# Optimization experiments

Measured on AMD Instinct MI355X. Metric: run time of the kernel, lower is better.

## Reference

```python
import jax, jax.numpy as jnp
import numpy as np

D_MODEL = 1024
NUM_HEADS = 16
D_K = D_MODEL // NUM_HEADS


def setup_inputs() -> dict:
    key = jax.random.key(0)
    ks = jax.random.split(key, 12)
    B, S = 2, 2048
    s = 1.0 / np.sqrt(D_MODEL)
    inp = {
        "query": jax.random.normal(ks[0], (B, S, D_MODEL), jnp.float32),
        "key": jax.random.normal(ks[1], (B, S, D_MODEL), jnp.float32),
        "value": jax.random.normal(ks[2], (B, S, D_MODEL), jnp.float32),
        "Wq": jax.random.normal(ks[3], (D_MODEL, D_MODEL), jnp.float32) * s,
        "bq": jax.random.normal(ks[4], (D_MODEL,), jnp.float32) * s,
        "Wk": jax.random.normal(ks[5], (D_MODEL, D_MODEL), jnp.float32) * s,
        "bk": jax.random.normal(ks[6], (D_MODEL,), jnp.float32) * s,
        "Wv": jax.random.normal(ks[7], (D_MODEL, D_MODEL), jnp.float32) * s,
        "bv": jax.random.normal(ks[8], (D_MODEL,), jnp.float32) * s,
        "Wo": jax.random.normal(ks[9], (D_MODEL, D_MODEL), jnp.float32) * s,
        "bo": jax.random.normal(ks[10], (D_MODEL,), jnp.float32) * s,
    }
    return inp


def _split_heads(x):
    B, S, _ = x.shape
    return x.reshape(B, S, NUM_HEADS, D_K).transpose(0, 2, 1, 3)  # [B,H,S,Dk]


def reference(query, key, value, Wq, bq, Wk, bk, Wv, bv, Wo, bo):
    # Linear projections (torch Linear: x @ W.T + b)
    Q = _split_heads(query @ Wq.T + bq)
    K = _split_heads(key @ Wk.T + bk)
    V = _split_heads(value @ Wv.T + bv)
    scale = 1.0 / jnp.sqrt(jnp.asarray(D_K, Q.dtype))
    scores = jnp.einsum('bhqd,bhkd->bhqk', Q, K) * scale  # [B,H,S,S]
    attn = jax.nn.softmax(scores, axis=-1)
    # dropout is identity in eval mode
    x = jnp.einsum('bhqk,bhkd->bhqd', attn, V)
    B, H, S, Dk = x.shape
    x = x.transpose(0, 2, 1, 3).reshape(B, S, H * Dk)
    return x @ Wo.T + bo
```

## Files before the change

kernel.cpp:

```cpp
#include <hip/hip_runtime.h>
#include <hip/hip_bf16.h>

typedef __bf16 bf16;
typedef __attribute__((ext_vector_type(4))) __bf16 bf16x4;
typedef __attribute__((ext_vector_type(8))) __bf16 bf16x8;
typedef __attribute__((ext_vector_type(4))) float f32x4;
typedef __attribute__((ext_vector_type(16))) float f32x16;
typedef unsigned int u32;

#define D_MODEL 1024
#define NHEADS 16
#define DK 64
#define BATCH 2
#define SEQ 2048
#define NTOK (BATCH * SEQ)

#define QSCALE 0.18033688011112042f
#define DEFER_THR 8.0f

__device__ __forceinline__ u32 cvtpk_bf16(float lo, float hi) {
  u32 r;
  asm("v_cvt_pk_bf16_f32 %0, %1, %2" : "=v"(r) : "v"(lo), "v"(hi));
  return r;
}
__device__ __forceinline__ void plswap(u32& a, u32& b) {
  asm("v_permlane32_swap_b32 %0, %1" : "+v"(a), "+v"(b));
}
__device__ __forceinline__ float fast_exp2(float x) {
#if __has_builtin(__builtin_amdgcn_exp2f)
  return __builtin_amdgcn_exp2f(x);
#else
  return exp2f(x);
#endif
}
__device__ __forceinline__ float xhalf_max(float x) {
  return fmaxf(x, __shfl_xor(x, 32));
}
__device__ __forceinline__ float xhalf_add(float x) {
  return x + __shfl_xor(x, 32);
}

__device__ __forceinline__ int frag_off_q(int s, int d) {
  return ((s >> 5) << 11) + ((d >> 4) << 9) + ((((d >> 3) & 1) * 32 + (s & 31)) << 3) + (d & 7);
}
__device__ __forceinline__ int frag_off_k(int s, int d) {
  return ((s >> 6) << 12) + ((((s >> 5) & 1) * 4 + (d >> 4)) << 9) +
         ((((d >> 3) & 1) * 32 + (s & 31)) << 3) + (d & 7);
}
__device__ __forceinline__ int frag_off_v(int s, int d) {
  return ((s >> 6) << 12) + (((d >> 5) * 4 + ((s >> 4) & 3)) << 9) +
         ((((s >> 3) & 1) * 32 + (d & 31)) << 3) + (s & 7);
}

__global__ __launch_bounds__(256) void cvt3_kernel(
    const float* __restrict__ s0, const float* __restrict__ s1, const float* __restrict__ s2,
    bf16* __restrict__ d0, bf16* __restrict__ d1, bf16* __restrict__ d2, int n4) {
  int i = blockIdx.x * blockDim.x + threadIdx.x;
  if (i >= n4) return;
  const float* s = blockIdx.y == 0 ? s0 : blockIdx.y == 1 ? s1 : s2;
  bf16* d = blockIdx.y == 0 ? d0 : blockIdx.y == 1 ? d1 : d2;
  float4 v = reinterpret_cast<const float4*>(s)[i];
  bf16x4 o;
  o[0] = (bf16)v.x; o[1] = (bf16)v.y; o[2] = (bf16)v.z; o[3] = (bf16)v.w;
  reinterpret_cast<bf16x4*>(d)[i] = o;
}

__global__ __launch_bounds__(256) void cvt4_kernel(
    const float* __restrict__ s0, const float* __restrict__ s1,
    const float* __restrict__ s2, const float* __restrict__ s3,
    bf16* __restrict__ d0, bf16* __restrict__ d1, bf16* __restrict__ d2, bf16* __restrict__ d3,
    int n4) {
  int i = blockIdx.x * blockDim.x + threadIdx.x;
  if (i >= n4) return;
  const float* s = blockIdx.y == 0 ? s0 : blockIdx.y == 1 ? s1 : blockIdx.y == 2 ? s2 : s3;
  bf16* d = blockIdx.y == 0 ? d0 : blockIdx.y == 1 ? d1 : blockIdx.y == 2 ? d2 : d3;
  float4 v = reinterpret_cast<const float4*>(s)[i];
  bf16x4 o;
  o[0] = (bf16)v.x; o[1] = (bf16)v.y; o[2] = (bf16)v.z; o[3] = (bf16)v.w;
  reinterpret_cast<bf16x4*>(d)[i] = o;
}

#define ASYNC_COPY16(gptr, lptr)                                                \
  __builtin_amdgcn_global_load_lds(                                             \
      (__attribute__((address_space(1))) void*)(gptr),                          \
      (__attribute__((address_space(3))) void*)(lptr), 16, 0, 0)

struct ProjArgs {
  const bf16* A[3];
  const bf16* W[3];
  const float* bias[3];
  bf16* out[3];
};

__global__ __launch_bounds__(256) void gemm_proj(ProjArgs pa, int K) {
  __shared__ bf16 As[128][32];
  __shared__ bf16 Bs[128][32];
  const int z = blockIdx.z;
  const bf16* A = pa.A[z];
  const bf16* Bw = pa.W[z];
  const int m0 = blockIdx.x * 128;
  const int n0 = blockIdx.y * 128;

  const int t = threadIdx.x;
  const int wave = t >> 6;
  const int lane = t & 63;
  const int wr = (wave >> 1) * 64;
  const int wc = (wave & 1) * 64;
  const int r4 = lane >> 2;
  const int c8 = (lane & 3) * 8;
  const int fr = lane & 15;
  const int fk = (lane >> 4) * 8;

  f32x4 acc[4][4] = {};

  for (int k0 = 0; k0 < K; k0 += 32) {
    ASYNC_COPY16(&A[(size_t)(m0 + wave * 16 + r4) * K + k0 + c8], &As[wave * 16][0]);
    ASYNC_COPY16(&A[(size_t)(m0 + 64 + wave * 16 + r4) * K + k0 + c8], &As[64 + wave * 16][0]);
    ASYNC_COPY16(&Bw[(size_t)(n0 + wave * 16 + r4) * K + k0 + c8], &Bs[wave * 16][0]);
    ASYNC_COPY16(&Bw[(size_t)(n0 + 64 + wave * 16 + r4) * K + k0 + c8], &Bs[64 + wave * 16][0]);
    __syncthreads();

    bf16x8 af[4], bfr[4];
#pragma unroll
    for (int m = 0; m < 4; m++)
      af[m] = *reinterpret_cast<const bf16x8*>(&As[wr + m * 16 + fr][fk]);
#pragma unroll
    for (int n = 0; n < 4; n++)
      bfr[n] = *reinterpret_cast<const bf16x8*>(&Bs[wc + n * 16 + fr][fk]);
#pragma unroll
    for (int m = 0; m < 4; m++)
#pragma unroll
      for (int n = 0; n < 4; n++)
        acc[m][n] = __builtin_amdgcn_mfma_f32_16x16x32_bf16(af[m], bfr[n], acc[m][n], 0, 0, 0);
    __syncthreads();
  }

  const float scale = (z == 0) ? QSCALE : 1.0f;
  const float* bias = pa.bias[z];
  bf16* out = pa.out[z];
#pragma unroll
  for (int m = 0; m < 4; m++) {
#pragma unroll
    for (int n = 0; n < 4; n++) {
      const int col = n0 + wc + n * 16 + fr;
      const float bv = bias[col];
#pragma unroll
      for (int j = 0; j < 4; j++) {
        const int row = m0 + wr + m * 16 + (lane >> 4) * 4 + j;
        const float v = (acc[m][n][j] + bv) * scale;
        const int b = row >> 11;
        const int s = row & (SEQ - 1);
        const int h = col >> 6;
        const int d = col & (DK - 1);
        const size_t base = (size_t)(b * NHEADS + h) * SEQ * DK;
        int off;
        if (z == 0)      off = frag_off_q(s, d);
        else if (z == 1) off = frag_off_k(s, d);
        else             off = frag_off_v(s, d);
        out[base + off] = (bf16)v;
      }
    }
  }
}

__global__ __launch_bounds__(256) void gemm_out(
    const bf16* __restrict__ A, const bf16* __restrict__ Bw,
    const float* __restrict__ bias, float* __restrict__ out, int K) {
  __shared__ bf16 As[128][32];
  __shared__ bf16 Bs[128][32];
  const int m0 = blockIdx.x * 128;
  const int n0 = blockIdx.y * 128;

  const int t = threadIdx.x;
  const int wave = t >> 6;
  const int lane = t & 63;
  const int wr = (wave >> 1) * 64;
  const int wc = (wave & 1) * 64;
  const int r4 = lane >> 2;
  const int c8 = (lane & 3) * 8;
  const int fr = lane & 15;
  const int fk = (lane >> 4) * 8;

  f32x4 acc[4][4] = {};

  for (int k0 = 0; k0 < K; k0 += 32) {
    ASYNC_COPY16(&A[(size_t)(m0 + wave * 16 + r4) * K + k0 + c8], &As[wave * 16][0]);
    ASYNC_COPY16(&A[(size_t)(m0 + 64 + wave * 16 + r4) * K + k0 + c8], &As[64 + wave * 16][0]);
    ASYNC_COPY16(&Bw[(size_t)(n0 + wave * 16 + r4) * K + k0 + c8], &Bs[wave * 16][0]);
    ASYNC_COPY16(&Bw[(size_t)(n0 + 64 + wave * 16 + r4) * K + k0 + c8], &Bs[64 + wave * 16][0]);
    __syncthreads();

    bf16x8 af[4], bfr[4];
#pragma unroll
    for (int m = 0; m < 4; m++)
      af[m] = *reinterpret_cast<const bf16x8*>(&As[wr + m * 16 + fr][fk]);
#pragma unroll
    for (int n = 0; n < 4; n++)
      bfr[n] = *reinterpret_cast<const bf16x8*>(&Bs[wc + n * 16 + fr][fk]);
#pragma unroll
    for (int m = 0; m < 4; m++)
#pragma unroll
      for (int n = 0; n < 4; n++)
        acc[m][n] = __builtin_amdgcn_mfma_f32_16x16x32_bf16(af[m], bfr[n], acc[m][n], 0, 0, 0);
    __syncthreads();
  }

#pragma unroll
  for (int m = 0; m < 4; m++) {
#pragma unroll
    for (int n = 0; n < 4; n++) {
      const int col = n0 + wc + n * 16 + fr;
      const float bv = bias[col];
#pragma unroll
      for (int j = 0; j < 4; j++) {
        const int row = m0 + wr + m * 16 + (lane >> 4) * 4 + j;
        out[(size_t)row * D_MODEL + col] = acc[m][n][j] + bv;
      }
    }
  }
}

#define QBLK 32
#define KVBLK 32
#define NT (SEQ / KVBLK)

__global__ __launch_bounds__(256, 2) void attn_kernel(
    const bf16* __restrict__ Qf,
    const bf16* __restrict__ Kf,
    const bf16* __restrict__ Vf,
    bf16* __restrict__ X) {
  const int lane = threadIdx.x & 63;
  const int wave = threadIdx.x >> 6;

  const int i = blockIdx.x;
  const int xcd = i & 7;
  const int slot = i >> 3;
  const int hgrp = slot >> 4;
  const int xq = slot & 15;
  const int bh = xcd + 8 * hgrp;
  const int bb = bh >> 4, hh = bh & (NHEADS - 1);
  const int q0 = xq * (QBLK * 4) + wave * QBLK;
  const int row = lane & 31, hi = lane >> 5;

  const bf16* Qp = Qf + (size_t)bh * SEQ * DK + (size_t)q0 * DK;
  const bf16* Kp = Kf + (size_t)bh * SEQ * DK;
  const bf16* Vp = Vf + (size_t)bh * SEQ * DK;

  bf16x8 qf[4];
#pragma unroll
  for (int kd = 0; kd < 4; kd++)
    qf[kd] = *reinterpret_cast<const bf16x8*>(&Qp[kd * 512 + lane * 8]);

  f32x16 ot0, ot1;
#pragma unroll
  for (int r = 0; r < 16; r++) { ot0[r] = 0.f; ot1[r] = 0.f; }
  float m_run = -1e30f, l_run = 0.f;

  bf16x8 ka[4], kb[4];

#define LOADK32(dst, tt)                                                        \
  {                                                                             \
    const bf16* kbase_ = Kp + (size_t)(tt) * 2048 + lane * 8;                   \
    _Pragma("unroll") for (int kd = 0; kd < 4; kd++)                            \
        dst[kd] = *reinterpret_cast<const bf16x8*>(&kbase_[kd * 512]);          \
  }

  LOADK32(ka, 0)
  LOADK32(kb, 1)
  f32x16 sa, sb;
#pragma unroll
  for (int r = 0; r < 16; r++) sa[r] = 0.f;
  __builtin_amdgcn_s_setprio(1);
#pragma unroll
  for (int kd = 0; kd < 4; kd++)
    sa = __builtin_amdgcn_mfma_f32_32x32x16_bf16(ka[kd], qf[kd], sa, 0, 0, 0);
  __builtin_amdgcn_s_setprio(0);

  auto pipe = [&](f32x16& SC, f32x16& SN, bf16x8 (&KN)[4], bf16x8 (&KL)[4], int tc) {
#pragma unroll
    for (int r = 0; r < 16; r++) SN[r] = 0.f;
    __builtin_amdgcn_s_setprio(1);
#pragma unroll
    for (int kd = 0; kd < 4; kd++)
      SN = __builtin_amdgcn_mfma_f32_32x32x16_bf16(KN[kd], qf[kd], SN, 0, 0, 0);
    __builtin_amdgcn_s_setprio(0);

    LOADK32(KL, (tc + 2) & (NT - 1))

    bf16x8 vf[2][2];
    {
      const bf16* vbase_ = Vp + (size_t)(tc >> 1) * 4096 + lane * 8;
      const int so = (tc & 1) * 2;
#pragma unroll
      for (int dh = 0; dh < 2; dh++)
#pragma unroll
        for (int ks = 0; ks < 2; ks++)
          vf[dh][ks] = *reinterpret_cast<const bf16x8*>(
              &vbase_[(dh * 4 + so + ks) * 512]);
    }

    float w8[8];
#pragma unroll
    for (int r = 0; r < 8; r++) w8[r] = fmaxf(SC[r], SC[r + 8]);
#pragma unroll
    for (int r = 0; r < 4; r++) w8[r] = fmaxf(w8[r], w8[r + 4]);
    float mx = fmaxf(fmaxf(w8[0], w8[1]), fmaxf(w8[2], w8[3]));
    mx = xhalf_max(mx);
    if (__any(mx > m_run + DEFER_THR)) {
      const float mn = fmaxf(m_run, mx);
      const float alpha = fast_exp2(m_run - mn);
      m_run = mn;
      l_run *= alpha;
#pragma unroll
      for (int r = 0; r < 16; r++) { ot0[r] *= alpha; ot1[r] *= alpha; }
    }
    float p[16];
#pragma unroll
    for (int r = 0; r < 16; r++) p[r] = fast_exp2(SC[r] - m_run);
    float a8[8];
#pragma unroll
    for (int r = 0; r < 8; r++) a8[r] = p[r] + p[r + 8];
#pragma unroll
    for (int r = 0; r < 4; r++) a8[r] += a8[r + 4];
    float rs = (a8[0] + a8[1]) + (a8[2] + a8[3]);
    l_run += xhalf_add(rs);

    u32 c[8];
#pragma unroll
    for (int i2 = 0; i2 < 8; i2++) c[i2] = cvtpk_bf16(p[2 * i2], p[2 * i2 + 1]);
    plswap(c[0], c[2]);   plswap(c[1], c[3]);
    plswap(c[4], c[6]);   plswap(c[5], c[7]);
    bf16x8 pbv[2];
#pragma unroll
    for (int ks = 0; ks < 2; ks++) {
      union { u32 u[4]; bf16x8 v; } pk;
      pk.u[0] = c[ks * 4 + 0]; pk.u[1] = c[ks * 4 + 1];
      pk.u[2] = c[ks * 4 + 2]; pk.u[3] = c[ks * 4 + 3];
      pbv[ks] = pk.v;
    }

    __builtin_amdgcn_s_setprio(1);
    ot0 = __builtin_amdgcn_mfma_f32_32x32x16_bf16(vf[0][0], pbv[0], ot0, 0, 0, 0);
    ot0 = __builtin_amdgcn_mfma_f32_32x32x16_bf16(vf[0][1], pbv[1], ot0, 0, 0, 0);
    ot1 = __builtin_amdgcn_mfma_f32_32x32x16_bf16(vf[1][0], pbv[0], ot1, 0, 0, 0);
    ot1 = __builtin_amdgcn_mfma_f32_32x32x16_bf16(vf[1][1], pbv[1], ot1, 0, 0, 0);
    __builtin_amdgcn_s_setprio(0);
  };

  for (int t = 0; t < NT; t += 2) {
    pipe(sa, sb, kb, ka, t);
    pipe(sb, sa, ka, kb, t + 1);
  }

  const float inv = 1.0f / l_run;
  bf16* Xp = X + ((size_t)bb * SEQ + q0 + row) * D_MODEL + hh * DK;
#pragma unroll
  for (int g = 0; g < 4; g++) {
    bf16x4 w0, w1;
#pragma unroll
    for (int j = 0; j < 4; j++) {
      w0[j] = (bf16)(ot0[g * 4 + j] * inv);
      w1[j] = (bf16)(ot1[g * 4 + j] * inv);
    }
    *reinterpret_cast<bf16x4*>(&Xp[g * 8 + hi * 4]) = w0;
    *reinterpret_cast<bf16x4*>(&Xp[32 + g * 8 + hi * 4]) = w1;
  }
}

extern "C" void kernel_launch(void* const* d_in, const int* in_sizes, int n_in,
                              void* d_out, int out_size, void* d_ws, size_t ws_size,
                              hipStream_t stream) {
  const float* q  = (const float*)d_in[0];
  const float* k  = (const float*)d_in[1];
  const float* v  = (const float*)d_in[2];
  const float* Wq = (const float*)d_in[3];
  const float* bq = (const float*)d_in[4];
  const float* Wk = (const float*)d_in[5];
  const float* bk = (const float*)d_in[6];
  const float* Wv = (const float*)d_in[7];
  const float* bv = (const float*)d_in[8];
  const float* Wo = (const float*)d_in[9];
  const float* bo = (const float*)d_in[10];

  char* ws = (char*)d_ws;
  size_t off = 0;
  auto alloc = [&](size_t bytes) -> void* {
    void* p = ws + off;
    off += (bytes + 255) & ~(size_t)255;
    return p;
  };
  const size_t ACT = (size_t)NTOK * D_MODEL;
  const size_t WEL = (size_t)D_MODEL * D_MODEL;

  bf16* Xq  = (bf16*)alloc(ACT * 2);
  bf16* Xk  = (bf16*)alloc(ACT * 2);
  bf16* Xv  = (bf16*)alloc(ACT * 2);
  bf16* Wqb = (bf16*)alloc(WEL * 2);
  bf16* Wkb = (bf16*)alloc(WEL * 2);
  bf16* Wvb = (bf16*)alloc(WEL * 2);
  bf16* Wob = (bf16*)alloc(WEL * 2);
  bf16* Qfb = (bf16*)alloc(ACT * 2);
  bf16* Kfb = (bf16*)alloc(ACT * 2);
  bf16* Vfb = (bf16*)alloc(ACT * 2);
  bf16* Xa  = (bf16*)alloc(ACT * 2);

  {
    int n4 = (int)(ACT / 4);
    cvt3_kernel<<<dim3((n4 + 255) / 256, 3), dim3(256), 0, stream>>>(q, k, v, Xq, Xk, Xv, n4);
  }
  {
    int n4 = (int)(WEL / 4);
    cvt4_kernel<<<dim3((n4 + 255) / 256, 4), dim3(256), 0, stream>>>(
        Wq, Wk, Wv, Wo, Wqb, Wkb, Wvb, Wob, n4);
  }

  ProjArgs pa;
  pa.A[0] = Xq;  pa.A[1] = Xk;  pa.A[2] = Xv;
  pa.W[0] = Wqb; pa.W[1] = Wkb; pa.W[2] = Wvb;
  pa.bias[0] = bq; pa.bias[1] = bk; pa.bias[2] = bv;
  pa.out[0] = Qfb; pa.out[1] = Kfb; pa.out[2] = Vfb;
  gemm_proj<<<dim3(NTOK / 128, D_MODEL / 128, 3), dim3(256), 0, stream>>>(pa, D_MODEL);

  attn_kernel<<<dim3(512), dim3(256), 0, stream>>>(Qfb, Kfb, Vfb, Xa);

  gemm_out<<<dim3(NTOK / 128, D_MODEL / 128), dim3(256), 0, stream>>>(
      Xa, Wob, bo, (float*)d_out, D_MODEL);
}
```

Baseline: 138.2 us.

## Split KV range across two waves per query block and merge through LDS

The attention kernel moves from four waves each owning a 32-row query block to two waves sharing one query block. Each wave processes alternate KV tiles, and the partial softmax states (max, sum, output) are combined through shared memory at the end. This launches four times as many smaller blocks, giving more parallelism and letting the two halves of the KV stream be read concurrently. It also starts m_run at zero, computes exp before the deferred rescale (then rescales p), and postpones the cross-half row-sum reduction until after the loop. The costs are an LDS merge step with a barrier and numerics that assume scores stay within the deferral threshold of zero.

```diff
diff --git a/kernel.cpp b/kernel.cpp
--- a/kernel.cpp
+++ b/kernel.cpp
@@ -223,23 +223,27 @@
 #define QBLK 32
 #define KVBLK 32
 #define NT (SEQ / KVBLK)
-
-__global__ __launch_bounds__(256, 2) void attn_kernel(
+#define NLOC (NT / 2)
+
+__global__ __launch_bounds__(128, 2) void attn_kernel(
     const bf16* __restrict__ Qf,
     const bf16* __restrict__ Kf,
     const bf16* __restrict__ Vf,
     bf16* __restrict__ X) {
+  __shared__ float lds_o[32][64];
+  __shared__ float lds_ml[2][64];
+
   const int lane = threadIdx.x & 63;
   const int wave = threadIdx.x >> 6;
 
   const int i = blockIdx.x;
   const int xcd = i & 7;
   const int slot = i >> 3;
-  const int hgrp = slot >> 4;
-  const int xq = slot & 15;
+  const int hgrp = slot >> 6;
+  const int qb = slot & 63;
   const int bh = xcd + 8 * hgrp;
   const int bb = bh >> 4, hh = bh & (NHEADS - 1);
-  const int q0 = xq * (QBLK * 4) + wave * QBLK;
+  const int q0 = qb * QBLK;
   const int row = lane & 31, hi = lane >> 5;
 
   const bf16* Qp = Qf + (size_t)bh * SEQ * DK + (size_t)q0 * DK;
@@ -251,10 +255,10 @@
   for (int kd = 0; kd < 4; kd++)
     qf[kd] = *reinterpret_cast<const bf16x8*>(&Qp[kd * 512 + lane * 8]);
 
-  f32x16 ot0, ot1;
-#pragma unroll
-  for (int r = 0; r < 16; r++) { ot0[r] = 0.f; ot1[r] = 0.f; }
-  float m_run = -1e30f, l_run = 0.f;
+  f32x16 ot0, ot1, fz;
+#pragma unroll
+  for (int r = 0; r < 16; r++) { ot0[r] = 0.f; ot1[r] = 0.f; fz[r] = 0.f; }
+  float m_run = 0.f, l_run = 0.f;
 
   bf16x8 ka[4], kb[4];
 
@@ -265,27 +269,28 @@
         dst[kd] = *reinterpret_cast<const bf16x8*>(&kbase_[kd * 512]);          \
   }
 
-  LOADK32(ka, 0)
-  LOADK32(kb, 1)
+  auto gt = [&](int li) { return wave + 2 * (li & (NLOC - 1)); };
+
+  LOADK32(ka, gt(0))
+  LOADK32(kb, gt(1))
   f32x16 sa, sb;
-#pragma unroll
-  for (int r = 0; r < 16; r++) sa[r] = 0.f;
   __builtin_amdgcn_s_setprio(1);
-#pragma unroll
-  for (int kd = 0; kd < 4; kd++)
+  sa = __builtin_amdgcn_mfma_f32_32x32x16_bf16(ka[0], qf[0], fz, 0, 0, 0);
+#pragma unroll
+  for (int kd = 1; kd < 4; kd++)
     sa = __builtin_amdgcn_mfma_f32_32x32x16_bf16(ka[kd], qf[kd], sa, 0, 0, 0);
   __builtin_amdgcn_s_setprio(0);
 
-  auto pipe = [&](f32x16& SC, f32x16& SN, bf16x8 (&KN)[4], bf16x8 (&KL)[4], int tc) {
-#pragma unroll
-    for (int r = 0; r < 16; r++) SN[r] = 0.f;
+  auto pipe = [&](f32x16& SC, f32x16& SN, bf16x8 (&KN)[4], bf16x8 (&KL)[4],
+                  int tc, int tp) {
     __builtin_amdgcn_s_setprio(1);
-#pragma unroll
-    for (int kd = 0; kd < 4; kd++)
+    SN = __builtin_amdgcn_mfma_f32_32x32x16_bf16(KN[0], qf[0], fz, 0, 0, 0);
+#pragma unroll
+    for (int kd = 1; kd < 4; kd++)
       SN = __builtin_amdgcn_mfma_f32_32x32x16_bf16(KN[kd], qf[kd], SN, 0, 0, 0);
     __builtin_amdgcn_s_setprio(0);
 
-    LOADK32(KL, (tc + 2) & (NT - 1))
+    LOADK32(KL, tp)
 
     bf16x8 vf[2][2];
     {
@@ -299,6 +304,9 @@
               &vbase_[(dh * 4 + so + ks) * 512]);
     }
 
+    float p[16];
+#pragma unroll
+    for (int r = 0; r < 16; r++) p[r] = fast_exp2(SC[r] - m_run);
     float w8[8];
 #pragma unroll
     for (int r = 0; r < 8; r++) w8[r] = fmaxf(SC[r], SC[r + 8]);
@@ -312,18 +320,16 @@
       m_run = mn;
       l_run *= alpha;
 #pragma unroll
+      for (int r = 0; r < 16; r++) p[r] *= alpha;
+#pragma unroll
       for (int r = 0; r < 16; r++) { ot0[r] *= alpha; ot1[r] *= alpha; }
     }
-    float p[16];
-#pragma unroll
-    for (int r = 0; r < 16; r++) p[r] = fast_exp2(SC[r] - m_run);
     float a8[8];
 #pragma unroll
     for (int r = 0; r < 8; r++) a8[r] = p[r] + p[r + 8];
 #pragma unroll
     for (int r = 0; r < 4; r++) a8[r] += a8[r + 4];
-    float rs = (a8[0] + a8[1]) + (a8[2] + a8[3]);
-    l_run += xhalf_add(rs);
+    l_run += (a8[0] + a8[1]) + (a8[2] + a8[3]);
 
     u32 c[8];
 #pragma unroll
@@ -347,23 +353,42 @@
     __builtin_amdgcn_s_setprio(0);
   };
 
-  for (int t = 0; t < NT; t += 2) {
-    pipe(sa, sb, kb, ka, t);
-    pipe(sb, sa, ka, kb, t + 1);
-  }
-
-  const float inv = 1.0f / l_run;
-  bf16* Xp = X + ((size_t)bb * SEQ + q0 + row) * D_MODEL + hh * DK;
-#pragma unroll
-  for (int g = 0; g < 4; g++) {
-    bf16x4 w0, w1;
-#pragma unroll
-    for (int j = 0; j < 4; j++) {
-      w0[j] = (bf16)(ot0[g * 4 + j] * inv);
-      w1[j] = (bf16)(ot1[g * 4 + j] * inv);
-    }
-    *reinterpret_cast<bf16x4*>(&Xp[g * 8 + hi * 4]) = w0;
-    *reinterpret_cast<bf16x4*>(&Xp[32 + g * 8 + hi * 4]) = w1;
+  for (int li = 0; li < NLOC; li += 2) {
+    pipe(sa, sb, kb, ka, gt(li), gt(li + 2));
+    pipe(sb, sa, ka, kb, gt(li + 1), gt(li + 3));
+  }
+
+  l_run = xhalf_add(l_run);
+
+  if (wave == 1) {
+#pragma unroll
+    for (int r = 0; r < 16; r++) {
+      lds_o[r][lane] = ot0[r];
+      lds_o[16 + r][lane] = ot1[r];
+    }
+    lds_ml[0][lane] = m_run;
+    lds_ml[1][lane] = l_run;
+  }
+  __syncthreads();
+  if (wave == 0) {
+    const float m1 = lds_ml[0][lane];
+    const float l1 = lds_ml[1][lane];
+    const float mm = fmaxf(m_run, m1);
+    const float s0 = fast_exp2(m_run - mm);
+    const float s1 = fast_exp2(m1 - mm);
+    const float inv = 1.0f / (l_run * s0 + l1 * s1);
+    bf16* Xp = X + ((size_t)bb * SEQ + q0 + row) * D_MODEL + hh * DK;
+#pragma unroll
+    for (int g = 0; g < 4; g++) {
+      bf16x4 w0, w1;
+#pragma unroll
+      for (int j = 0; j < 4; j++) {
+        w0[j] = (bf16)((ot0[g * 4 + j] * s0 + lds_o[g * 4 + j][lane] * s1) * inv);
+        w1[j] = (bf16)((ot1[g * 4 + j] * s0 + lds_o[16 + g * 4 + j][lane] * s1) * inv);
+      }
+      *reinterpret_cast<bf16x4*>(&Xp[g * 8 + hi * 4]) = w0;
+      *reinterpret_cast<bf16x4*>(&Xp[32 + g * 8 + hi * 4]) = w1;
+    }
   }
 }
 
@@ -421,7 +446,7 @@
   pa.out[0] = Qfb; pa.out[1] = Kfb; pa.out[2] = Vfb;
   gemm_proj<<<dim3(NTOK / 128, D_MODEL / 128, 3), dim3(256), 0, stream>>>(pa, D_MODEL);
 
-  attn_kernel<<<dim3(512), dim3(256), 0, stream>>>(Qfb, Kfb, Vfb, Xa);
+  attn_kernel<<<dim3(2048), dim3(128), 0, stream>>>(Qfb, Kfb, Vfb, Xa);
 
   gemm_out<<<dim3(NTOK / 128, D_MODEL / 128), dim3(256), 0, stream>>>(
       Xa, Wob, bo, (float*)d_out, D_MODEL);
```

New measurement: 148.5 us. +7.5%, slower.
